# Optimization experiments

Measured on AMD Instinct MI355X. Metric: run time of the kernel, lower is better.

The kernel has to match this reference:

```python
import math
import jax, jax.numpy as jnp
import numpy as np

D_MODEL = 2048
D_INNER = 4096   # expand * d_model
D_STATE = 16
D_CONV = 4
DT_RANK = 128    # d_model / 16
SCALE_X = 0.05         # conv1d input (int8) scale
SCALE_CONV_OUT = 0.05  # conv1d output (int8) scale


def quant(x, scale):
    """Simulated int8 quantize -> dequantize (as in the W4A8 pipeline)."""
    return jnp.clip(jnp.round(x / scale), -128.0, 127.0) * scale


def fwht(x):
    """Normalized fast Walsh-Hadamard transform over the last axis (power of 2)."""
    d = x.shape[-1]
    shp = x.shape
    x = x.reshape(-1, d)
    h = 1
    while h < d:
        x = x.reshape(-1, d // (2 * h), 2, h)
        a, s = x[:, :, 0, :], x[:, :, 1, :]
        x = jnp.stack([a + s, a - s], axis=2).reshape(-1, d)
        h *= 2
    return (x * (d ** -0.5)).reshape(shp)


def setup_inputs() -> dict:
    key = jax.random.key(0)
    ks = jax.random.split(key, 10)
    b, l = 2, 1024
    dt0 = jnp.exp(jax.random.uniform(ks[6], (D_INNER,), minval=math.log(1e-3), maxval=math.log(1e-1)))
    dt_bias = dt0 + jnp.log(-jnp.expm1(-dt0))  # inverse softplus of dt0
    A = -jnp.tile(jnp.arange(1.0, D_STATE + 1.0, dtype=jnp.float32), (D_INNER, 1))
    return {
        "hidden_states": jax.random.normal(ks[0], (b, l, D_MODEL), jnp.float32),
        "W_in": (jax.random.normal(ks[1], (2 * D_INNER, D_MODEL), jnp.float32) * 0.02),
        "conv_w": (jax.random.normal(ks[2], (D_INNER, D_CONV), jnp.float32) * 0.2),
        "conv_b": (jax.random.normal(ks[3], (D_INNER,), jnp.float32) * 0.02),
        "W_x": (jax.random.normal(ks[4], (DT_RANK + 2 * D_STATE, D_INNER), jnp.float32) * 0.02),
        "W_dt": (jax.random.normal(ks[5], (D_INNER, DT_RANK), jnp.float32) * 0.02),
        "dt_bias": dt_bias.astype(jnp.float32),
        "A": A.astype(jnp.float32),
        "D": jnp.ones((D_INNER,), jnp.float32),
        "W_out": (jax.random.normal(ks[7], (D_MODEL, D_INNER), jnp.float32) * 0.02),
    }


def reference(hidden_states, W_in, conv_w, conv_b, W_x, W_dt, dt_bias, A, D, W_out):
    b, l, dm = hidden_states.shape
    # in_proj -> seqlen-last layout, chunk into x (conv path) and z (gate)
    xz = jnp.einsum('bld,ed->bel', hidden_states, W_in)  # [b, 2*d_inner, l]
    x, z = jnp.split(xz, 2, axis=1)                      # [b, d_inner, l] each
    x = quant(x, SCALE_X)                                # int8 activation sim
    # fused causal depthwise conv1d + SiLU + requantize (quant_causal_conv1d)
    xp = jnp.pad(x, ((0, 0), (0, 0), (D_CONV - 1, 0)))
    xc = jax.lax.conv_general_dilated(
        xp, conv_w[:, None, :], (1,), 'VALID',
        dimension_numbers=('NCH', 'OIH', 'NCH'), feature_group_count=D_INNER)
    u = quant(jax.nn.silu(xc + conv_b[None, :, None]), SCALE_CONV_OUT)  # [b,d,l]
    # x_proj -> dt, B, C
    x_dbl = jnp.einsum('bdl,ed->ble', u, W_x)            # [b, l, dt_rank+2n]
    dt_in, B, C = jnp.split(x_dbl, [DT_RANK, DT_RANK + D_STATE], axis=-1)
    dt = jax.nn.softplus(jnp.einsum('blr,dr->bld', dt_in, W_dt) + dt_bias)  # [b,l,d]
    # selective scan: h_t = exp(dt*A) h_{t-1} + dt*B*u ; y = C.h + D*u
    xs = (dt.transpose(1, 0, 2),          # [l,b,d]
          u.transpose(2, 0, 1),           # [l,b,d]
          B.transpose(1, 0, 2),           # [l,b,n]
          C.transpose(1, 0, 2))           # [l,b,n]
    h0 = jnp.zeros((b, D_INNER, D_STATE), hidden_states.dtype)

    def step(h, inp):
        dt_t, u_t, B_t, C_t = inp
        dA = jnp.exp(dt_t[..., None] * A)                       # [b,d,n]
        h = dA * h + (dt_t * u_t)[..., None] * B_t[:, None, :]  # [b,d,n]
        return h, jnp.einsum('bdn,bn->bd', h, C_t)

    _, ys = jax.lax.scan(step, h0, xs)                    # ys: [l,b,d]
    y = ys.transpose(1, 2, 0) + D[:, None] * u            # [b,d,l]
    y = y * jax.nn.silu(z)                                # gated output
    y = fwht(y.transpose(0, 2, 1))                        # Hadamard over channels
    return jnp.einsum('ble,de->bld', y, W_out)            # out_proj -> [b,l,d_model]
```

## Files before the change

kernel.cpp:

```cpp
#include <hip/hip_runtime.h>
#include <math.h>

#define BB 2
#define LL 1024
#define DMODEL 2048
#define DI 4096
#define NSTATE 16
#define RANK 128
#define MM (BB*LL)
#define XE (2*DI)
#define EDBL (RANK + 2*NSTATE)
#define NWORDS (MM*DI/32)
#define NC 16
#define CL (LL/NC)

typedef __bf16 bf16x8 __attribute__((ext_vector_type(8)));
typedef __bf16 bf16x4 __attribute__((ext_vector_type(4)));
typedef float  f32x4  __attribute__((ext_vector_type(4)));

__device__ __forceinline__ float quant005(float x) {
    float q = rintf(x / 0.05f);
    q = fminf(fmaxf(q, -128.f), 127.f);
    return q * 0.05f;
}
__device__ __forceinline__ float softplusf(float x) {
    return fmaxf(x, 0.f) + log1pf(expf(-fabsf(x)));
}

__global__ __launch_bounds__(256) void reduce4_kernel(
    const float* __restrict__ p, float* __restrict__ out)
{
    const int gid = blockIdx.x * 256 + threadIdx.x;
    const size_t S = (size_t)MM * DMODEL;
    out[gid] = p[gid] + p[gid + S] + p[gid + 2 * S] + p[gid + 3 * S];
}

__global__ __launch_bounds__(256) void reduce6_kernel(
    const float* __restrict__ p, float* __restrict__ xdbl,
    __bf16* __restrict__ XdH, __bf16* __restrict__ XdM)
{
    const int gid = blockIdx.x * 256 + threadIdx.x;
    const size_t S = (size_t)MM * EDBL;
    float v = p[gid];
    #pragma unroll
    for (int s = 1; s < 6; ++s) v += p[gid + s * S];
    xdbl[gid] = v;
    const int m = gid / EDBL, e = gid - m * EDBL;
    if (e < RANK) {
        const __bf16 h = (__bf16)v;
        XdH[(size_t)m * RANK + e] = h;
        XdM[(size_t)m * RANK + e] = (__bf16)(v - (float)h);
    }
}

__global__ __launch_bounds__(256) void conv_kernel(
    const float* __restrict__ X, const float* __restrict__ conv_w,
    const float* __restrict__ conv_b, signed char* __restrict__ u8,
    __bf16* __restrict__ uh, __bf16* __restrict__ um)
{
    const int gid = blockIdx.x * 256 + threadIdx.x;
    const int bl = gid >> 12, d = gid & (DI - 1);
    const int l = bl & (LL - 1);
    const float4 w4 = *(const float4*)(conv_w + 4 * d);
    const float wk[4] = {w4.x, w4.y, w4.z, w4.w};
    float acc = 0.f;
    #pragma unroll
    for (int k = 0; k < 4; ++k) {
        const int lp = l - 3 + k;
        if (lp >= 0) acc = fmaf(X[(size_t)(bl - 3 + k) * XE + d], wk[k], acc);
    }
    const float v = acc + conv_b[d];
    const float s = v / (1.f + expf(-v));
    float qf = rintf(s / 0.05f);
    qf = fminf(fmaxf(qf, -128.f), 127.f);
    u8[gid] = (signed char)(int)qf;
    const float q = qf * 0.05f;
    const __bf16 h = (__bf16)q;
    uh[gid] = h;
    um[gid] = (__bf16)(q - (float)h);
}

__global__ __launch_bounds__(256) void scan_p1(
    const float* __restrict__ dtb, const signed char* __restrict__ u8,
    const float* __restrict__ xdbl,
    float* __restrict__ hend, float* __restrict__ S)
{
    const int bx = blockIdx.x;
    const int c  = bx & (NC - 1);
    const int dg = (bx >> 4) & 255;
    const int b  = bx >> 12;
    const int dl = threadIdx.x >> 4, n = threadIdx.x & 15;
    const int d  = (dg << 4) + dl;
    const int t0 = c * CL;
    const float* dtp = dtb + ((size_t)b * LL + t0) * DI + d;
    const signed char* up = u8 + ((size_t)b * LL + t0) * DI + d;
    const float* xe  = xdbl + ((size_t)b * LL + t0) * EDBL;
    const float An = -(float)(n + 1);
    float h = 0.f, s = 0.f;
    for (int t = 0; t < CL; ++t) {
        const float dt = dtp[(size_t)t * DI];
        const float uv = 0.05f * (float)up[(size_t)t * DI];
        const float Bn = xe[t * EDBL + RANK + n];
        const float w = __expf(dt * An);
        h = fmaf(h, w, dt * uv * Bn);
        s += dt;
    }
    hend[(((size_t)b * DI + d) * NC + c) * 16 + n] = h;
    if (n == 0) S[((size_t)b * DI + d) * NC + c] = s;
}

__global__ __launch_bounds__(256) void scan_p2(
    float* __restrict__ hend, const float* __restrict__ S)
{
    const int gid = blockIdx.x * 256 + threadIdx.x;
    const int n  = gid & 15;
    const int bd = gid >> 4;
    const float An = -(float)(n + 1);
    float* hp = hend + (size_t)bd * NC * 16 + n;
    const float* Sp = S + (size_t)bd * NC;
    float h = 0.f;
    for (int c = 0; c < NC; ++c) {
        const float he = hp[c * 16];
        const float P  = __expf(An * Sp[c]);
        hp[c * 16] = h;
        h = fmaf(h, P, he);
    }
}

__global__ __launch_bounds__(256) void scan_p3(
    const float* __restrict__ dtb, const signed char* __restrict__ u8,
    const float* __restrict__ xdbl, const float* __restrict__ Dvec,
    const float* __restrict__ hin, float* __restrict__ X)
{
    const int bx = blockIdx.x;
    const int c  = bx & (NC - 1);
    const int dg = (bx >> 4) & 255;
    const int b  = bx >> 12;
    const int dl = threadIdx.x >> 4, n = threadIdx.x & 15;
    const int d  = (dg << 4) + dl;
    const int t0 = c * CL;
    const float* dtp = dtb + ((size_t)b * LL + t0) * DI + d;
    const signed char* up = u8 + ((size_t)b * LL + t0) * DI + d;
    const float* xe  = xdbl + ((size_t)b * LL + t0) * EDBL;
    float* Xp = X + ((size_t)b * LL + t0) * XE + d;
    const float Dv = Dvec[d];
    const float An = -(float)(n + 1);
    float h = hin[(((size_t)b * DI + d) * NC + c) * 16 + n];
    for (int t = 0; t < CL; ++t) {
        const float dt = dtp[(size_t)t * DI];
        const float uv = 0.05f * (float)up[(size_t)t * DI];
        const float* e = xe + t * EDBL;
        const float Bn = e[RANK + n];
        const float Cn = e[RANK + NSTATE + n];
        const float w = __expf(dt * An);
        h = fmaf(h, w, dt * uv * Bn);
        float y = h * Cn;
        y += __shfl_xor(y, 1);
        y += __shfl_xor(y, 2);
        y += __shfl_xor(y, 4);
        y += __shfl_xor(y, 8);
        if (n == 0) {
            const float z = Xp[(size_t)t * XE + DI];
            const float sz = z / (1.f + __expf(-z));
            Xp[(size_t)t * XE] = (y + Dv * uv) * sz;
        }
    }
}

__device__ __forceinline__ void bfy8(float* a)
{
    float t;
    t = a[0]; a[0] = t + a[1]; a[1] = t - a[1];
    t = a[2]; a[2] = t + a[3]; a[3] = t - a[3];
    t = a[4]; a[4] = t + a[5]; a[5] = t - a[5];
    t = a[6]; a[6] = t + a[7]; a[7] = t - a[7];
    t = a[0]; a[0] = t + a[2]; a[2] = t - a[2];
    t = a[1]; a[1] = t + a[3]; a[3] = t - a[3];
    t = a[4]; a[4] = t + a[6]; a[6] = t - a[6];
    t = a[5]; a[5] = t + a[7]; a[7] = t - a[7];
    t = a[0]; a[0] = t + a[4]; a[4] = t - a[4];
    t = a[1]; a[1] = t + a[5]; a[5] = t - a[5];
    t = a[2]; a[2] = t + a[6]; a[6] = t - a[6];
    t = a[3]; a[3] = t + a[7]; a[7] = t - a[7];
}
#define FWIDX(a) ((a) + ((a) >> 5))

__global__ __launch_bounds__(512) void fwht8_kernel(
    float* __restrict__ X, __bf16* __restrict__ XhC, __bf16* __restrict__ XmC)
{
    __shared__ float s[DI + DI / 32];
    const int tid = threadIdx.x;
    float* base = X + (size_t)blockIdx.x * XE;
    {
        float a[8];
        const float4 v0 = *(const float4*)(base + tid * 8);
        const float4 v1 = *(const float4*)(base + tid * 8 + 4);
        a[0] = v0.x; a[1] = v0.y; a[2] = v0.z; a[3] = v0.w;
        a[4] = v1.x; a[5] = v1.y; a[6] = v1.z; a[7] = v1.w;
        bfy8(a);
        const int p = FWIDX(tid * 8);
        *(float4*)(s + p)     = make_float4(a[0], a[1], a[2], a[3]);
        *(float4*)(s + p + 4) = make_float4(a[4], a[5], a[6], a[7]);
    }
    __syncthreads();
    {
        const int b = (tid >> 3) * 64 + (tid & 7);
        float a[8];
        #pragma unroll
        for (int j = 0; j < 8; ++j) a[j] = s[FWIDX(b + j * 8)];
        bfy8(a);
        #pragma unroll
        for (int j = 0; j < 8; ++j) s[FWIDX(b + j * 8)] = a[j];
    }
    __syncthreads();
    {
        const int b = (tid >> 6) * 512 + (tid & 63);
        float a[8];
        #pragma unroll
        for (int j = 0; j < 8; ++j) a[j] = s[FWIDX(b + j * 64)];
        bfy8(a);
        #pragma unroll
        for (int j = 0; j < 8; ++j) s[FWIDX(b + j * 64)] = a[j];
    }
    __syncthreads();
    {
        const int b = tid;
        float a[8];
        #pragma unroll
        for (int j = 0; j < 8; ++j) a[j] = s[FWIDX(b + j * 512)];
        bfy8(a);
        #pragma unroll
        for (int j = 0; j < 8; ++j) s[FWIDX(b + j * 512)] = a[j];
    }
    __syncthreads();
    const float sc = 1.f / 64.f;
    __bf16* Xh = XhC + (size_t)blockIdx.x * DI;
    __bf16* Xm = XmC + (size_t)blockIdx.x * DI;
    {
        const int i = tid * 8;
        const float* sp = s + FWIDX(i);
        bf16x8 hv, mv;
        #pragma unroll
        for (int j = 0; j < 8; ++j) {
            const float v = sp[j] * sc;
            const __bf16 h = (__bf16)v;
            hv[j] = h;
            mv[j] = (__bf16)(v - (float)h);
        }
        *(bf16x8*)&Xh[i] = hv;
        *(bf16x8*)&Xm[i] = mv;
    }
}

__global__ __launch_bounds__(256) void splitw_kernel(
    const float* __restrict__ W, __bf16* __restrict__ H, __bf16* __restrict__ L)
{
    const int gid = blockIdx.x * 256 + threadIdx.x;
    const float4 a = *(const float4*)(W + (size_t)gid * 4);
    const float af[4] = {a.x, a.y, a.z, a.w};
    bf16x4 h, l;
    #pragma unroll
    for (int i = 0; i < 4; ++i) {
        const __bf16 hh = (__bf16)af[i];
        h[i] = hh;
        l[i] = (__bf16)(af[i] - (float)hh);
    }
    *(bf16x4*)&H[(size_t)gid * 4] = h;
    *(bf16x4*)&L[(size_t)gid * 4] = l;
}

__global__ __launch_bounds__(256) void splitwx_kernel(
    const float* __restrict__ W, __bf16* __restrict__ H, __bf16* __restrict__ L)
{
    const int gid = blockIdx.x * 256 + threadIdx.x;
    const int row = gid >> 10, c4 = (gid & 1023) << 2;
    float4 a = make_float4(0.f, 0.f, 0.f, 0.f);
    if (row < EDBL) a = *(const float4*)(W + (size_t)row * DI + c4);
    const float af[4] = {a.x, a.y, a.z, a.w};
    bf16x4 h, l;
    #pragma unroll
    for (int i = 0; i < 4; ++i) {
        const __bf16 hh = (__bf16)af[i];
        h[i] = hh;
        l[i] = (__bf16)(af[i] - (float)hh);
    }
    *(bf16x4*)&H[(size_t)(row * DI + c4)] = h;
    *(bf16x4*)&L[(size_t)(row * DI + c4)] = l;
}

__global__ __launch_bounds__(256) void zeromask_kernel(unsigned* __restrict__ mask)
{
    const int gid = blockIdx.x * 256 + threadIdx.x;
    mask[gid] = 0u;
}

__device__ __forceinline__ void stage_tile(const __bf16* __restrict__ g, int ld,
                                           __bf16* lds, int tid)
{
    const int r = tid >> 2;
    const int c = (tid & 3) << 3;
    #pragma unroll
    for (int i = 0; i < 2; ++i) {
        const __bf16* src = g + (size_t)(r + i * 64) * ld + c;
        __builtin_amdgcn_global_load_lds(
            (const __attribute__((address_space(1))) void*)src,
            (__attribute__((address_space(3))) void*)(lds + (r + i * 64) * 32 + c),
            16, 0, 0);
    }
}

template<int EPI>
__global__ __launch_bounds__(256) void gemm3k(
    const __bf16* __restrict__ Ah, const __bf16* __restrict__ Am, int lda,
    const __bf16* __restrict__ Bh, const __bf16* __restrict__ Bm, int ldb,
    float* __restrict__ C, int N, int ldc, int K, int Kz,
    const float* __restrict__ bias)
{
    if (EPI == 2) C += (size_t)blockIdx.z * MM * ldc;
    __shared__ __bf16 sA[128 * 32];
    __shared__ __bf16 sB[128 * 32];
    const int tid  = threadIdx.x;
    const int lane = tid & 63, w = tid >> 6;
    const int wr = w >> 1, wc = w & 1;
    const int bm = blockIdx.y << 7, bn = blockIdx.x << 7;
    const int lr = lane & 15;
    const int kg = (lane >> 4) << 3;
    const int kbeg = blockIdx.z * Kz;

    f32x4 acc[4][4] = {};
    for (int k0 = kbeg; k0 < kbeg + Kz; k0 += 32) {
        const __bf16* Ap; const __bf16* Bp; int kk;
        if (k0 < K)          { Ap = Ah; Bp = Bh; kk = k0; }
        else if (k0 < 2 * K) { Ap = Ah; Bp = Bm; kk = k0 - K; }
        else                 { Ap = Am; Bp = Bh; kk = k0 - 2 * K; }
        stage_tile(Ap + (size_t)bm * lda + kk, lda, sA, tid);
        stage_tile(Bp + (size_t)bn * ldb + kk, ldb, sB, tid);
        __syncthreads();
        bf16x8 a[4], b[4];
        #pragma unroll
        for (int f = 0; f < 4; ++f) {
            a[f] = *(const bf16x8*)&sA[(wr * 64 + f * 16 + lr) * 32 + kg];
            b[f] = *(const bf16x8*)&sB[(wc * 64 + f * 16 + lr) * 32 + kg];
        }
        #pragma unroll
        for (int i = 0; i < 4; ++i)
            #pragma unroll
            for (int j = 0; j < 4; ++j)
                acc[i][j] = __builtin_amdgcn_mfma_f32_16x16x32_bf16(a[i], b[j], acc[i][j], 0, 0, 0);
        __syncthreads();
    }
    #pragma unroll
    for (int i = 0; i < 4; ++i)
        #pragma unroll
        for (int j = 0; j < 4; ++j) {
            const int col  = bn + wc * 64 + j * 16 + (lane & 15);
            const int row0 = bm + wr * 64 + i * 16 + (lane >> 4) * 4;
            #pragma unroll
            for (int r = 0; r < 4; ++r) {
                float v = acc[i][j][r];
                if (EPI == 4) v = softplusf(v + bias[col]);
                if (EPI != 2 || col < N)
                    C[(size_t)(row0 + r) * ldc + col] = v;
            }
        }
}

__device__ __forceinline__ void plane_sel2(int kt, int ktps,
    const __bf16* A0h, const __bf16* A0m, const __bf16* B0h, const __bf16* B0m,
    const __bf16*& Ap, const __bf16*& Bp, int& kc)
{
    if (kt < ktps)          { Ap = A0h; Bp = B0h; kc = kt * 64; }
    else if (kt < 2 * ktps) { Ap = A0h; Bp = B0m; kc = (kt - ktps) * 64; }
    else                    { Ap = A0m; Bp = B0h; kc = (kt - 2 * ktps) * 64; }
}

__device__ __forceinline__ int swz_off(int row, int l16)
{
    const int off = row * 32 + l16 * 8;
    return off ^ (((off >> 6) & 3) << 3);
}

__device__ __forceinline__ void stage_h(
    const __bf16* __restrict__ baseP, const int* goff, int kcol,
    __bf16* ldsHalf, const int* ldso)
{
    #pragma unroll
    for (int i = 0; i < 2; ++i)
        __builtin_amdgcn_global_load_lds(
            (const __attribute__((address_space(1))) void*)(baseP + goff[i] + kcol),
            (__attribute__((address_space(3))) void*)(ldsHalf + ldso[i]),
            16, 0, 0);
}

#define G1BAR  asm volatile("s_barrier" ::: "memory")
#define G1LGKM asm volatile("s_waitcnt lgkmcnt(0)" ::: "memory")
#define G1MFMA(N0, N1)                                                            \
    __builtin_amdgcn_s_setprio(1);                                                \
    _Pragma("unroll")                                                             \
    for (int f = 0; f < 8; ++f) {                                                 \
        acc[f][N0] = __builtin_amdgcn_mfma_f32_16x16x32_bf16(a[f], b0, acc[f][N0], 0, 0, 0); \
        acc[f][N1] = __builtin_amdgcn_mfma_f32_16x16x32_bf16(a[f], b1, acc[f][N1], 0, 0, 0); \
    }                                                                             \
    __builtin_amdgcn_s_setprio(0)

template<int EPI>
__global__ __launch_bounds__(512, 2) void gemm_8p(
    const __bf16* __restrict__ Ah, const __bf16* __restrict__ Am, int lda,
    const __bf16* __restrict__ Bh, const __bf16* __restrict__ Bm, int ldb,
    float* __restrict__ C0, int ktps, unsigned* __restrict__ mask)
{
    __shared__ __bf16 lds[2][2][2][8192];
    const int tid = threadIdx.x;
    const int lane = tid & 63, w = tid >> 6;
    const int wr = w >> 2, wc = w & 3;
    const int lr = lane & 15, l16 = lane >> 4;
    const int T = 3 * ktps;

    const int nwg = gridDim.x * gridDim.y * gridDim.z;
    int flat = ((int)blockIdx.z * gridDim.y + blockIdx.y) * gridDim.x + blockIdx.x;
    flat = (flat & 7) * (nwg >> 3) + (flat >> 3);
    const int bxs = flat % gridDim.x;
    const int tzy = flat / gridDim.x;
    const int bys = tzy % gridDim.y;
    const int bzs = tzy / gridDim.y;
    const int bm = bys << 8, bn = bxs << 8;
    const int zoff = (EPI == 2) ? bzs * 1024 : 0;

    const __bf16* A0h = Ah + (size_t)bm * lda;
    const __bf16* A0m = Am + (size_t)bm * lda;
    const __bf16* B0h = Bh + (size_t)bn * ldb;
    const __bf16* B0m = Bm + (size_t)bn * ldb;

    int ga[2], gb[2], lo[2];
    #pragma unroll
    for (int i = 0; i < 2; ++i) {
        const int t = i * 512 + tid;
        const int row = t >> 2;
        const int gr = (t & 3) ^ ((t >> 3) & 3);
        ga[i] = row * lda + gr * 8;
        gb[i] = row * ldb + gr * 8;
        lo[i] = t * 8;
    }
    int sa[8], sb[4];
    #pragma unroll
    for (int f = 0; f < 8; ++f) sa[f] = swz_off(wr * 128 + f * 16 + lr, l16);
    #pragma unroll
    for (int nf = 0; nf < 4; ++nf) sb[nf] = swz_off(wc * 64 + nf * 16 + lr, l16);

    {
        const __bf16 *Ap, *Bp; int kc;
        plane_sel2(0, ktps, A0h, A0m, B0h, B0m, Ap, Bp, kc);
        stage_h(Ap, ga, zoff + kc +  0, (__bf16*)&lds[0][0][0][0], lo);
        stage_h(Bp, gb, zoff + kc +  0, (__bf16*)&lds[0][1][0][0], lo);
        stage_h(Ap, ga, zoff + kc + 32, (__bf16*)&lds[0][0][1][0], lo);
        stage_h(Bp, gb, zoff + kc + 32, (__bf16*)&lds[0][1][1][0], lo);
        plane_sel2(1, ktps, A0h, A0m, B0h, B0m, Ap, Bp, kc);
        stage_h(Ap, ga, zoff + kc +  0, (__bf16*)&lds[1][0][0][0], lo);
        stage_h(Bp, gb, zoff + kc +  0, (__bf16*)&lds[1][1][0][0], lo);
        stage_h(Ap, ga, zoff + kc + 32, (__bf16*)&lds[1][0][1][0], lo);
    }
    asm volatile("s_waitcnt vmcnt(6)" ::: "memory");
    G1BAR;

    f32x4 acc[8][4] = {};
    for (int kt = 0; kt < T; ++kt) {
        const int c = kt & 1;
        const __bf16* lA = &lds[c][0][0][0];
        const __bf16* lB = &lds[c][1][0][0];
        const __bf16 *Ap2, *Bp2; int kc2;
        plane_sel2(kt + 2 < T ? kt + 2 : T - 1, ktps, A0h, A0m, B0h, B0m, Ap2, Bp2, kc2);
        bf16x8 a[8], b0, b1;

        #pragma unroll
        for (int f = 0; f < 8; ++f) a[f] = *(const bf16x8*)(lA + sa[f]);
        b0 = *(const bf16x8*)(lB + sb[0]);
        b1 = *(const bf16x8*)(lB + sb[1]);
        if (kt + 1 < T) {
            const __bf16 *Ap1, *Bp1; int kc1;
            plane_sel2(kt + 1, ktps, A0h, A0m, B0h, B0m, Ap1, Bp1, kc1);
            stage_h(Bp1, gb, zoff + kc1 + 32, (__bf16*)&lds[c ^ 1][1][1][0], lo);
        }
        G1BAR; G1LGKM;
        G1MFMA(0, 1);
        G1BAR;

        b0 = *(const bf16x8*)(lB + sb[2]);
        b1 = *(const bf16x8*)(lB + sb[3]);
        if (kt + 2 < T)
            stage_h(Ap2, ga, zoff + kc2, (__bf16*)&lds[c][0][0][0], lo);
        G1BAR; G1LGKM;
        G1MFMA(2, 3);
        G1BAR;

        #pragma unroll
        for (int f = 0; f < 8; ++f) a[f] = *(const bf16x8*)(lA + 8192 + sa[f]);
        b0 = *(const bf16x8*)(lB + 8192 + sb[0]);
        b1 = *(const bf16x8*)(lB + 8192 + sb[1]);
        if (kt + 2 < T)
            stage_h(Bp2, gb, zoff + kc2, (__bf16*)&lds[c][1][0][0], lo);
        G1BAR; G1LGKM;
        G1MFMA(0, 1);
        G1BAR;

        b0 = *(const bf16x8*)(lB + 8192 + sb[2]);
        b1 = *(const bf16x8*)(lB + 8192 + sb[3]);
        if (kt + 2 < T)
            stage_h(Ap2, ga, zoff + kc2 + 32, (__bf16*)&lds[c][0][1][0], lo);
        if (kt < T - 2) { asm volatile("s_waitcnt vmcnt(6)" ::: "memory"); }
        else            { asm volatile("s_waitcnt vmcnt(0)" ::: "memory"); }
        G1BAR; G1LGKM;
        G1MFMA(2, 3);
        G1BAR;
    }

    float* Cp; int ldc;
    if (EPI == 1) { Cp = C0; ldc = XE; }
    else          { Cp = C0 + (size_t)bzs * MM * DMODEL; ldc = DMODEL; }
    #pragma unroll
    for (int f = 0; f < 8; ++f)
        #pragma unroll
        for (int nf = 0; nf < 4; ++nf) {
            const int col  = bn + wc * 64 + nf * 16 + lr;
            const int row0 = bm + wr * 128 + f * 16 + l16 * 4;
            #pragma unroll
            for (int r = 0; r < 4; ++r) {
                float v = acc[f][nf][r];
                const int row = row0 + r;
                if (EPI == 1 && col < DI) {
                    const float fq = v / 0.05f;
                    const float q = rintf(fq);
                    if (0.5f - fabsf(fq - q) < 1e-3f) {
                        const int e = row * DI + col;
                        atomicOr(&mask[e >> 5], 1u << (e & 31));
                    }
                    v = fminf(fmaxf(q, -128.f), 127.f) * 0.05f;
                }
                Cp[(size_t)row * ldc + col] = v;
            }
        }
}

__global__ __launch_bounds__(256) void fixup_kernel(
    const float* __restrict__ hidden, const float* __restrict__ W_in,
    const unsigned* __restrict__ mask, float* __restrict__ X)
{
    const int gwave = (blockIdx.x * 256 + threadIdx.x) >> 6;
    const int lane  = threadIdx.x & 63;
    const int nwaves = gridDim.x * 4;
    for (int base = gwave * 64; base < NWORDS; base += nwaves * 64) {
        const unsigned myw = mask[base + lane];
        unsigned long long bal = __ballot(myw != 0u);
        while (bal) {
            const int src = __ffsll((unsigned long long)bal) - 1;
            bal &= bal - 1;
            unsigned word = __shfl(myw, src);
            const int widx = base + src;
            while (word) {
                const int bit = __ffs(word) - 1;
                word &= word - 1;
                const int e = widx * 32 + bit;
                const int m = e >> 12, n = e & (DI - 1);
                const float* ap = hidden + (size_t)m * DMODEL;
                const float* bp = W_in   + (size_t)n * DMODEL;
                float s = 0.f;
                #pragma unroll
                for (int kk = 0; kk < 8; ++kk) {
                    const int k = kk * 256 + lane * 4;
                    const float4 a = *(const float4*)(ap + k);
                    const float4 b = *(const float4*)(bp + k);
                    s += a.x * b.x + a.y * b.y + a.z * b.z + a.w * b.w;
                }
                s += __shfl_xor(s, 1);  s += __shfl_xor(s, 2);  s += __shfl_xor(s, 4);
                s += __shfl_xor(s, 8);  s += __shfl_xor(s, 16); s += __shfl_xor(s, 32);
                if (lane == 0) X[(size_t)m * XE + n] = quant005(s);
            }
        }
    }
}

extern "C" void kernel_launch(void* const* d_in, const int* in_sizes, int n_in,
                              void* d_out, int out_size, void* d_ws, size_t ws_size,
                              hipStream_t stream)
{
    const float* hidden  = (const float*)d_in[0];
    const float* W_in    = (const float*)d_in[1];
    const float* conv_w  = (const float*)d_in[2];
    const float* conv_b  = (const float*)d_in[3];
    const float* W_x     = (const float*)d_in[4];
    const float* W_dt    = (const float*)d_in[5];
    const float* dt_bias = (const float*)d_in[6];
    const float* Dvec    = (const float*)d_in[8];
    const float* W_out   = (const float*)d_in[9];
    float* out = (float*)d_out;

    float* X    = (float*)d_ws;
    float* u    = X + (size_t)MM * XE;
    float* xdbl = u + (size_t)MM * DI;
    float* dtb  = xdbl + (size_t)MM * EDBL;
    __bf16* WinH  = (__bf16*)u;
    __bf16* WinM  = (__bf16*)dtb;
    unsigned* mask = (unsigned*)xdbl;
    signed char* u8 = (signed char*)u;
    __bf16* uh = (__bf16*)dtb;
    __bf16* um = uh + (size_t)MM * DI;
    __bf16* WoutH = (__bf16*)dtb;
    __bf16* WoutM = WoutH + (size_t)DMODEL * DI;
    __bf16* XhC = (__bf16*)u;
    __bf16* XmC = XhC + (size_t)MM * DI;
    float*  part4 = X;
    char* ob = (char*)d_out;
    __bf16* HinH = (__bf16*)ob;
    __bf16* HinM = HinH + (size_t)MM * DMODEL;
    __bf16* WxH  = (__bf16*)ob;
    __bf16* WxM  = WxH + (size_t)256 * DI;
    __bf16* WdtH = (__bf16*)(ob + ((size_t)4 << 20));
    __bf16* WdtM = WdtH + (size_t)DI * RANK;
    __bf16* XdH  = (__bf16*)(ob + ((size_t)6 << 20));
    __bf16* XdM  = XdH + (size_t)MM * RANK;
    float*  xpart = (float*)(ob + ((size_t)7 << 20));
    float* hend = (float*)ob;
    float* Ssum = hend + (size_t)BB * DI * NC * 16;

    splitw_kernel<<<2 * DI * DMODEL / 4 / 256, 256, 0, stream>>>(W_in, WinH, WinM);
    splitw_kernel<<<MM * DMODEL / 4 / 256, 256, 0, stream>>>(hidden, HinH, HinM);
    zeromask_kernel<<<NWORDS / 256, 256, 0, stream>>>(mask);
    gemm_8p<1><<<dim3(XE / 256, MM / 256), 512, 0, stream>>>(
        HinH, HinM, DMODEL, WinH, WinM, DMODEL, X, 32, mask);
    fixup_kernel<<<256, 256, 0, stream>>>(hidden, W_in, mask, X);
    splitwx_kernel<<<256 * DI / 4 / 256, 256, 0, stream>>>(W_x, WxH, WxM);
    splitw_kernel<<<DI * RANK / 4 / 256, 256, 0, stream>>>(W_dt, WdtH, WdtM);
    conv_kernel<<<MM * DI / 256, 256, 0, stream>>>(X, conv_w, conv_b, u8, uh, um);
    gemm3k<2><<<dim3(2, MM / 128, 6), 256, 0, stream>>>(
        uh, um, DI, WxH, WxM, DI, xpart, EDBL, EDBL, DI, 2048, nullptr);
    reduce6_kernel<<<MM * EDBL / 256, 256, 0, stream>>>(xpart, xdbl, XdH, XdM);
    gemm3k<4><<<dim3(DI / 128, MM / 128, 1), 256, 0, stream>>>(
        XdH, XdM, RANK, WdtH, WdtM, RANK, dtb, DI, DI, RANK, 3 * RANK, dt_bias);
    scan_p1<<<BB * 256 * NC, 256, 0, stream>>>(dtb, u8, xdbl, hend, Ssum);
    scan_p2<<<BB * DI * 16 / 256, 256, 0, stream>>>(hend, Ssum);
    scan_p3<<<BB * 256 * NC, 256, 0, stream>>>(dtb, u8, xdbl, Dvec, hend, X);
    fwht8_kernel<<<MM, 512, 0, stream>>>(X, XhC, XmC);
    splitw_kernel<<<DMODEL * DI / 4 / 256, 256, 0, stream>>>(W_out, WoutH, WoutM);
    gemm_8p<2><<<dim3(DMODEL / 256, MM / 256, 4), 512, 0, stream>>>(
        XhC, XmC, DI, WoutH, WoutM, DI, part4, 16, nullptr);
    reduce4_kernel<<<MM * DMODEL / 256, 256, 0, stream>>>(part4, out);
}
```

Measured before the change: 759.3 us.

## Prefetch A fragments across MFMA phases and split x/z buffers into dense planes

The main bf16-split GEMM now loads its A fragments from LDS one phase ahead into two register sets (aP/aQ), so those reads overlap the preceding MFMA batch, and the explicit lgkmcnt waits are dropped. The XCD-aware block-index swizzle is removed in favour of plain blockIdx mapping. The in_proj output is written to separate contiguous Xq and Z buffers with a DI stride instead of one interleaved XE-stride buffer, which tightens access strides for conv, scan_p3 and fwht. This costs extra registers (launch bounds 512,2), may lose L2 locality from the dropped swizzle, and relies on compiler-inserted waits for LDS correctness.

```diff
diff --git a/kernel.cpp b/kernel.cpp
--- a/kernel.cpp
+++ b/kernel.cpp
@@ -54,7 +54,7 @@
 }
 
 __global__ __launch_bounds__(256) void conv_kernel(
-    const float* __restrict__ X, const float* __restrict__ conv_w,
+    const float* __restrict__ Xq, const float* __restrict__ conv_w,
     const float* __restrict__ conv_b, signed char* __restrict__ u8,
     __bf16* __restrict__ uh, __bf16* __restrict__ um)
 {
@@ -67,7 +67,7 @@
     #pragma unroll
     for (int k = 0; k < 4; ++k) {
         const int lp = l - 3 + k;
-        if (lp >= 0) acc = fmaf(X[(size_t)(bl - 3 + k) * XE + d], wk[k], acc);
+        if (lp >= 0) acc = fmaf(Xq[(size_t)(bl - 3 + k) * DI + d], wk[k], acc);
     }
     const float v = acc + conv_b[d];
     const float s = v / (1.f + expf(-v));
@@ -130,7 +130,8 @@
 __global__ __launch_bounds__(256) void scan_p3(
     const float* __restrict__ dtb, const signed char* __restrict__ u8,
     const float* __restrict__ xdbl, const float* __restrict__ Dvec,
-    const float* __restrict__ hin, float* __restrict__ X)
+    const float* __restrict__ hin, const float* __restrict__ Z,
+    float* __restrict__ Xq)
 {
     const int bx = blockIdx.x;
     const int c  = bx & (NC - 1);
@@ -142,7 +143,8 @@
     const float* dtp = dtb + ((size_t)b * LL + t0) * DI + d;
     const signed char* up = u8 + ((size_t)b * LL + t0) * DI + d;
     const float* xe  = xdbl + ((size_t)b * LL + t0) * EDBL;
-    float* Xp = X + ((size_t)b * LL + t0) * XE + d;
+    const float* Zp  = Z  + ((size_t)b * LL + t0) * DI + d;
+    float* Yp        = Xq + ((size_t)b * LL + t0) * DI + d;
     const float Dv = Dvec[d];
     const float An = -(float)(n + 1);
     float h = hin[(((size_t)b * DI + d) * NC + c) * 16 + n];
@@ -160,9 +162,9 @@
         y += __shfl_xor(y, 4);
         y += __shfl_xor(y, 8);
         if (n == 0) {
-            const float z = Xp[(size_t)t * XE + DI];
+            const float z = Zp[(size_t)t * DI];
             const float sz = z / (1.f + __expf(-z));
-            Xp[(size_t)t * XE] = (y + Dv * uv) * sz;
+            Yp[(size_t)t * DI] = (y + Dv * uv) * sz;
         }
     }
 }
@@ -186,11 +188,11 @@
 #define FWIDX(a) ((a) + ((a) >> 5))
 
 __global__ __launch_bounds__(512) void fwht8_kernel(
-    float* __restrict__ X, __bf16* __restrict__ XhC, __bf16* __restrict__ XmC)
+    const float* __restrict__ Xq, __bf16* __restrict__ XhC, __bf16* __restrict__ XmC)
 {
     __shared__ float s[DI + DI / 32];
     const int tid = threadIdx.x;
-    float* base = X + (size_t)blockIdx.x * XE;
+    const float* base = Xq + (size_t)blockIdx.x * DI;
     {
         float a[8];
         const float4 v0 = *(const float4*)(base + tid * 8);
@@ -393,13 +395,12 @@
 }
 
 #define G1BAR  asm volatile("s_barrier" ::: "memory")
-#define G1LGKM asm volatile("s_waitcnt lgkmcnt(0)" ::: "memory")
-#define G1MFMA(N0, N1)                                                            \
+#define G1MFMA(AV, N0, N1)                                                        \
     __builtin_amdgcn_s_setprio(1);                                                \
     _Pragma("unroll")                                                             \
     for (int f = 0; f < 8; ++f) {                                                 \
-        acc[f][N0] = __builtin_amdgcn_mfma_f32_16x16x32_bf16(a[f], b0, acc[f][N0], 0, 0, 0); \
-        acc[f][N1] = __builtin_amdgcn_mfma_f32_16x16x32_bf16(a[f], b1, acc[f][N1], 0, 0, 0); \
+        acc[f][N0] = __builtin_amdgcn_mfma_f32_16x16x32_bf16(AV[f], b0, acc[f][N0], 0, 0, 0); \
+        acc[f][N1] = __builtin_amdgcn_mfma_f32_16x16x32_bf16(AV[f], b1, acc[f][N1], 0, 0, 0); \
     }                                                                             \
     __builtin_amdgcn_s_setprio(0)
 
@@ -407,24 +408,17 @@
 __global__ __launch_bounds__(512, 2) void gemm_8p(
     const __bf16* __restrict__ Ah, const __bf16* __restrict__ Am, int lda,
     const __bf16* __restrict__ Bh, const __bf16* __restrict__ Bm, int ldb,
-    float* __restrict__ C0, int ktps, unsigned* __restrict__ mask)
+    float* __restrict__ C0, float* __restrict__ C1,
+    int ktps, unsigned* __restrict__ mask)
 {
     __shared__ __bf16 lds[2][2][2][8192];
     const int tid = threadIdx.x;
     const int lane = tid & 63, w = tid >> 6;
     const int wr = w >> 2, wc = w & 3;
+    const int bm = blockIdx.y << 8, bn = blockIdx.x << 8;
     const int lr = lane & 15, l16 = lane >> 4;
     const int T = 3 * ktps;
-
-    const int nwg = gridDim.x * gridDim.y * gridDim.z;
-    int flat = ((int)blockIdx.z * gridDim.y + blockIdx.y) * gridDim.x + blockIdx.x;
-    flat = (flat & 7) * (nwg >> 3) + (flat >> 3);
-    const int bxs = flat % gridDim.x;
-    const int tzy = flat / gridDim.x;
-    const int bys = tzy % gridDim.y;
-    const int bzs = tzy / gridDim.y;
-    const int bm = bys << 8, bn = bxs << 8;
-    const int zoff = (EPI == 2) ? bzs * 1024 : 0;
+    const int zoff = (EPI == 2) ? (int)blockIdx.z * 1024 : 0;
 
     const __bf16* A0h = Ah + (size_t)bm * lda;
     const __bf16* A0m = Am + (size_t)bm * lda;
@@ -462,17 +456,20 @@
     asm volatile("s_waitcnt vmcnt(6)" ::: "memory");
     G1BAR;
 
+    bf16x8 aP[8], aQ[8];
+    #pragma unroll
+    for (int f = 0; f < 8; ++f) aP[f] = *(const bf16x8*)(&lds[0][0][0][0] + sa[f]);
+
     f32x4 acc[8][4] = {};
     for (int kt = 0; kt < T; ++kt) {
         const int c = kt & 1;
-        const __bf16* lA = &lds[c][0][0][0];
-        const __bf16* lB = &lds[c][1][0][0];
+        const __bf16* lA  = &lds[c][0][0][0];
+        const __bf16* lAn = &lds[c ^ 1][0][0][0];
+        const __bf16* lB  = &lds[c][1][0][0];
         const __bf16 *Ap2, *Bp2; int kc2;
         plane_sel2(kt + 2 < T ? kt + 2 : T - 1, ktps, A0h, A0m, B0h, B0m, Ap2, Bp2, kc2);
-        bf16x8 a[8], b0, b1;
-
-        #pragma unroll
-        for (int f = 0; f < 8; ++f) a[f] = *(const bf16x8*)(lA + sa[f]);
+        bf16x8 b0, b1;
+
         b0 = *(const bf16x8*)(lB + sb[0]);
         b1 = *(const bf16x8*)(lB + sb[1]);
         if (kt + 1 < T) {
@@ -480,26 +477,26 @@
             plane_sel2(kt + 1, ktps, A0h, A0m, B0h, B0m, Ap1, Bp1, kc1);
             stage_h(Bp1, gb, zoff + kc1 + 32, (__bf16*)&lds[c ^ 1][1][1][0], lo);
         }
-        G1BAR; G1LGKM;
-        G1MFMA(0, 1);
+        G1BAR;
+        G1MFMA(aP, 0, 1);
         G1BAR;
 
         b0 = *(const bf16x8*)(lB + sb[2]);
         b1 = *(const bf16x8*)(lB + sb[3]);
+        #pragma unroll
+        for (int f = 0; f < 8; ++f) aQ[f] = *(const bf16x8*)(lA + 8192 + sa[f]);
         if (kt + 2 < T)
             stage_h(Ap2, ga, zoff + kc2, (__bf16*)&lds[c][0][0][0], lo);
-        G1BAR; G1LGKM;
-        G1MFMA(2, 3);
-        G1BAR;
-
-        #pragma unroll
-        for (int f = 0; f < 8; ++f) a[f] = *(const bf16x8*)(lA + 8192 + sa[f]);
+        G1BAR;
+        G1MFMA(aP, 2, 3);
+        G1BAR;
+
         b0 = *(const bf16x8*)(lB + 8192 + sb[0]);
         b1 = *(const bf16x8*)(lB + 8192 + sb[1]);
         if (kt + 2 < T)
             stage_h(Bp2, gb, zoff + kc2, (__bf16*)&lds[c][1][0][0], lo);
-        G1BAR; G1LGKM;
-        G1MFMA(0, 1);
+        G1BAR;
+        G1MFMA(aQ, 0, 1);
         G1BAR;
 
         b0 = *(const bf16x8*)(lB + 8192 + sb[2]);
@@ -508,14 +505,13 @@
             stage_h(Ap2, ga, zoff + kc2 + 32, (__bf16*)&lds[c][0][1][0], lo);
         if (kt < T - 2) { asm volatile("s_waitcnt vmcnt(6)" ::: "memory"); }
         else            { asm volatile("s_waitcnt vmcnt(0)" ::: "memory"); }
-        G1BAR; G1LGKM;
-        G1MFMA(2, 3);
-        G1BAR;
-    }
-
-    float* Cp; int ldc;
-    if (EPI == 1) { Cp = C0; ldc = XE; }
-    else          { Cp = C0 + (size_t)bzs * MM * DMODEL; ldc = DMODEL; }
+        G1BAR;
+        #pragma unroll
+        for (int f = 0; f < 8; ++f) aP[f] = *(const bf16x8*)(lAn + sa[f]);
+        G1MFMA(aQ, 2, 3);
+        G1BAR;
+    }
+
     #pragma unroll
     for (int f = 0; f < 8; ++f)
         #pragma unroll
@@ -526,23 +522,30 @@
             for (int r = 0; r < 4; ++r) {
                 float v = acc[f][nf][r];
                 const int row = row0 + r;
-                if (EPI == 1 && col < DI) {
-                    const float fq = v / 0.05f;
-                    const float q = rintf(fq);
-                    if (0.5f - fabsf(fq - q) < 1e-3f) {
-                        const int e = row * DI + col;
-                        atomicOr(&mask[e >> 5], 1u << (e & 31));
+                if (EPI == 1) {
+                    if (col < DI) {
+                        const float fq = v / 0.05f;
+                        const float q = rintf(fq);
+                        if (0.5f - fabsf(fq - q) < 1e-3f) {
+                            const int e = row * DI + col;
+                            atomicOr(&mask[e >> 5], 1u << (e & 31));
+                        }
+                        v = fminf(fmaxf(q, -128.f), 127.f) * 0.05f;
+                        C0[(size_t)row * DI + col] = v;
+                    } else {
+                        C1[(size_t)row * DI + (col - DI)] = v;
                     }
-                    v = fminf(fmaxf(q, -128.f), 127.f) * 0.05f;
+                } else {
+                    float* Cp = C0 + (size_t)blockIdx.z * MM * DMODEL;
+                    Cp[(size_t)row * DMODEL + col] = v;
                 }
-                Cp[(size_t)row * ldc + col] = v;
             }
         }
 }
 
 __global__ __launch_bounds__(256) void fixup_kernel(
     const float* __restrict__ hidden, const float* __restrict__ W_in,
-    const unsigned* __restrict__ mask, float* __restrict__ X)
+    const unsigned* __restrict__ mask, float* __restrict__ Xq)
 {
     const int gwave = (blockIdx.x * 256 + threadIdx.x) >> 6;
     const int lane  = threadIdx.x & 63;
@@ -572,7 +575,7 @@
                 }
                 s += __shfl_xor(s, 1);  s += __shfl_xor(s, 2);  s += __shfl_xor(s, 4);
                 s += __shfl_xor(s, 8);  s += __shfl_xor(s, 16); s += __shfl_xor(s, 32);
-                if (lane == 0) X[(size_t)m * XE + n] = quant005(s);
+                if (lane == 0) Xq[(size_t)m * DI + n] = quant005(s);
             }
         }
     }
@@ -593,8 +596,9 @@
     const float* W_out   = (const float*)d_in[9];
     float* out = (float*)d_out;
 
-    float* X    = (float*)d_ws;
-    float* u    = X + (size_t)MM * XE;
+    float* Xq   = (float*)d_ws;
+    float* Z    = Xq + (size_t)MM * DI;
+    float* u    = Z + (size_t)MM * DI;
     float* xdbl = u + (size_t)MM * DI;
     float* dtb  = xdbl + (size_t)MM * EDBL;
     __bf16* WinH  = (__bf16*)u;
@@ -607,7 +611,7 @@
     __bf16* WoutM = WoutH + (size_t)DMODEL * DI;
     __bf16* XhC = (__bf16*)u;
     __bf16* XmC = XhC + (size_t)MM * DI;
-    float*  part4 = X;
+    float*  part4 = Xq;
     char* ob = (char*)d_out;
     __bf16* HinH = (__bf16*)ob;
     __bf16* HinM = HinH + (size_t)MM * DMODEL;
@@ -625,11 +629,11 @@
     splitw_kernel<<<MM * DMODEL / 4 / 256, 256, 0, stream>>>(hidden, HinH, HinM);
     zeromask_kernel<<<NWORDS / 256, 256, 0, stream>>>(mask);
     gemm_8p<1><<<dim3(XE / 256, MM / 256), 512, 0, stream>>>(
-        HinH, HinM, DMODEL, WinH, WinM, DMODEL, X, 32, mask);
-    fixup_kernel<<<256, 256, 0, stream>>>(hidden, W_in, mask, X);
+        HinH, HinM, DMODEL, WinH, WinM, DMODEL, Xq, Z, 32, mask);
+    fixup_kernel<<<256, 256, 0, stream>>>(hidden, W_in, mask, Xq);
     splitwx_kernel<<<256 * DI / 4 / 256, 256, 0, stream>>>(W_x, WxH, WxM);
     splitw_kernel<<<DI * RANK / 4 / 256, 256, 0, stream>>>(W_dt, WdtH, WdtM);
-    conv_kernel<<<MM * DI / 256, 256, 0, stream>>>(X, conv_w, conv_b, u8, uh, um);
+    conv_kernel<<<MM * DI / 256, 256, 0, stream>>>(Xq, conv_w, conv_b, u8, uh, um);
     gemm3k<2><<<dim3(2, MM / 128, 6), 256, 0, stream>>>(
         uh, um, DI, WxH, WxM, DI, xpart, EDBL, EDBL, DI, 2048, nullptr);
     reduce6_kernel<<<MM * EDBL / 256, 256, 0, stream>>>(xpart, xdbl, XdH, XdM);
@@ -637,10 +641,10 @@
         XdH, XdM, RANK, WdtH, WdtM, RANK, dtb, DI, DI, RANK, 3 * RANK, dt_bias);
     scan_p1<<<BB * 256 * NC, 256, 0, stream>>>(dtb, u8, xdbl, hend, Ssum);
     scan_p2<<<BB * DI * 16 / 256, 256, 0, stream>>>(hend, Ssum);
-    scan_p3<<<BB * 256 * NC, 256, 0, stream>>>(dtb, u8, xdbl, Dvec, hend, X);
-    fwht8_kernel<<<MM, 512, 0, stream>>>(X, XhC, XmC);
+    scan_p3<<<BB * 256 * NC, 256, 0, stream>>>(dtb, u8, xdbl, Dvec, hend, Z, Xq);
+    fwht8_kernel<<<MM, 512, 0, stream>>>(Xq, XhC, XmC);
     splitw_kernel<<<DMODEL * DI / 4 / 256, 256, 0, stream>>>(W_out, WoutH, WoutM);
     gemm_8p<2><<<dim3(DMODEL / 256, MM / 256, 4), 512, 0, stream>>>(
-        XhC, XmC, DI, WoutH, WoutM, DI, part4, 16, nullptr);
+        XhC, XmC, DI, WoutH, WoutM, DI, part4, nullptr, 16, nullptr);
     reduce4_kernel<<<MM * DMODEL / 256, 256, 0, stream>>>(part4, out);
 }
```

New measurement: 764.5 us. About the same (+0.7%).
